# Optimization experiments

Hardware: AMD Instinct MI355X
Metric: run time of the kernel (lower is better)

## Reference

```python
import jax, jax.numpy as jnp
import numpy as np

EPS = 1e-5

def headwise_linear(x, w):
    # x: [B,S,D], w: [NH, DH_out, DH_in] block-diagonal linear per head
    B, S, D = x.shape
    NH, O, DH = w.shape
    xh = x.reshape(B, S, NH, DH)
    return jnp.einsum('bshd,hod->bsho', xh, w).reshape(B, S, NH * O)

def setup_inputs() -> dict:
    key = jax.random.key(0)
    ks = jax.random.split(key, 10)
    B, S, D, NH, K = 8, 4096, 768, 4, 4
    DH = D // NH
    small = (2.0 / (5.0 * D)) ** 0.5  # small_init scale
    return {
        'x': jax.random.normal(ks[0], (B, S, D), jnp.float32),
        'conv_w': jax.random.normal(ks[1], (D, 1, K), jnp.float32) * (1.0 / K ** 0.5),
        'conv_b': jnp.zeros((D,), jnp.float32),
        'w_f': jax.random.normal(ks[2], (NH, DH, DH), jnp.float32) * small,
        'w_i': jax.random.normal(ks[3], (NH, DH, DH), jnp.float32) * small,
        'w_z': jax.random.normal(ks[4], (NH, DH, DH), jnp.float32) * small,
        'w_o': jax.random.normal(ks[5], (NH, DH, DH), jnp.float32) * small,
        'r_kernel': jax.random.normal(ks[6], (NH, DH, 4, DH), jnp.float32) * (1.0 / DH ** 0.5),
        'r_bias': jnp.zeros((4, NH, DH), jnp.float32),
        'gn_weight': jnp.ones((D,), jnp.float32),
    }

def reference(x, conv_w, conv_b, w_f, w_i, w_z, w_o, r_kernel, r_bias, gn_weight):
    B, S, D = x.shape
    NH, DH = r_kernel.shape[0], r_kernel.shape[1]
    K = conv_w.shape[-1]
    # --- causal depthwise conv1d + SiLU ---
    xt = jnp.transpose(x, (0, 2, 1))  # [B,D,S]
    xc = jax.lax.conv_general_dilated(xt, conv_w, (1,), [(K - 1, 0)],
                                      feature_group_count=D)
    x_conv = jax.nn.silu(jnp.transpose(xc + conv_b[None, :, None], (0, 2, 1)))
    # --- headwise gate projections (note: original code feeds fgate->i, igate->f) ---
    gi = headwise_linear(x_conv, w_f)
    gf = headwise_linear(x_conv, w_i)
    gz = headwise_linear(x, w_z)
    go = headwise_linear(x, w_o)
    Wx = jnp.stack([gi, gf, gz, go], axis=2).reshape(B, S, 4, NH, DH)
    Wx = jnp.transpose(Wx, (1, 0, 2, 3, 4))  # [S,B,4,NH,DH]
    # --- sLSTM recurrent scan with exponential gating + stabilizer m ---
    def step(carry, wx_t):
        y, c, n, m = carry  # each [B,NH,DH]
        Ry = jnp.einsum('bhd,hdge->bghe', y, r_kernel)  # [B,4,NH,DH]
        raw = wx_t + Ry + r_bias[None]
        iraw, fraw, zraw, oraw = raw[:, 0], raw[:, 1], raw[:, 2], raw[:, 3]
        logfplusm = m + jax.nn.log_sigmoid(fraw)
        mnew = jnp.maximum(iraw, logfplusm)
        igate = jnp.exp(iraw - mnew)
        fgate = jnp.exp(logfplusm - mnew)
        cnew = fgate * c + igate * jnp.tanh(zraw)
        nnew = fgate * n + igate
        ynew = jax.nn.sigmoid(oraw) * cnew / nnew
        return (ynew, cnew, nnew, mnew), ynew
    init = tuple(jnp.zeros((B, NH, DH), x.dtype) for _ in range(4))
    _, ys = jax.lax.scan(step, init, Wx)  # [S,B,NH,DH]
    y = jnp.transpose(ys, (1, 2, 0, 3))  # [B,NH,S,DH]
    # --- multi-head layer norm (group norm with NH groups over DH) ---
    mean = y.mean(-1, keepdims=True)
    var = y.var(-1, keepdims=True)
    yn = (y - mean) * jax.lax.rsqrt(var + EPS)
    yn = yn * gn_weight.reshape(1, NH, 1, DH)
    return jnp.transpose(yn, (0, 2, 1, 3)).reshape(B, S, NH * DH)
```

## Files before the change

### kernel.cpp

```cpp
#include <hip/hip_runtime.h>
#include <hip/hip_bf16.h>
#include <math.h>

#define B_ 8
#define S_ 4096
#define D_ 768
#define NH_ 4
#define DH_ 192
#define NTOT_ 768

typedef __attribute__((ext_vector_type(8))) short short8;
typedef __attribute__((ext_vector_type(4))) float floatx4;
typedef __attribute__((ext_vector_type(4))) short short4v;
typedef __attribute__((ext_vector_type(4))) unsigned int uint4v;
typedef _Float16 f16;

__device__ __forceinline__ short f2bs(float f) {
  union { float f; unsigned u; } v; v.f = f;
  unsigned r = v.u + 0x7FFFu + ((v.u >> 16) & 1u);
  return (short)(r >> 16);
}
__device__ __forceinline__ float bs2f(unsigned short s) {
  union { unsigned u; float f; } v; v.u = ((unsigned)s) << 16;
  return v.f;
}
__device__ __forceinline__ unsigned packh2(float lo, float hi) {
  union { f16 h[2]; unsigned u; } x;
  x.h[0] = (f16)lo; x.h[1] = (f16)hi;
  return x.u;
}

__device__ __forceinline__ float DOT2(unsigned r, unsigned y, float acc) {
  asm("v_dot2_f32_f16 %0, %1, %2, %0" : "+v"(acc) : "v"(r), "v"(y));
  return acc;
}

template<int CTRL>
__device__ __forceinline__ float qperm(float x) {
  return __int_as_float(__builtin_amdgcn_mov_dpp(__float_as_int(x), CTRL, 0xf, 0xf, true));
}

__global__ __launch_bounds__(256) void wconv_kernel(
    const float* __restrict__ wf, const float* __restrict__ wi,
    const float* __restrict__ wz, const float* __restrict__ wo,
    short* __restrict__ Wbf)
{
  int idx = blockIdx.x * 256 + threadIdx.x;
  int hg = idx / (DH_ * DH_);
  int r  = idx % (DH_ * DH_);
  int h = hg >> 2, g = hg & 3;
  const float* W = (g == 0) ? wf : (g == 1) ? wi : (g == 2) ? wz : wo;
  Wbf[idx] = f2bs(W[(size_t)h * DH_ * DH_ + r]);
}

__global__ __launch_bounds__(256) void conv_silu_kernel(
    const float* __restrict__ x, const float* __restrict__ cw, const float* __restrict__ cb,
    short* __restrict__ xb, short* __restrict__ xcb)
{
  const int b  = blockIdx.x / (S_ / 64);
  const int s0 = (blockIdx.x % (S_ / 64)) * 64;
  const int tid = threadIdx.x;
  float wv[3][4], bias[3], win[3][3];
  for (int j = 0; j < 3; ++j) {
    int d = tid + j * 256;
    for (int k = 0; k < 4; ++k) wv[j][k] = cw[d * 4 + k];
    bias[j] = cb[d];
    for (int p = 0; p < 3; ++p) {
      int s = s0 - 3 + p;
      win[j][p] = (s >= 0) ? x[((size_t)b * S_ + s) * D_ + d] : 0.f;
    }
  }
  for (int i = 0; i < 64; ++i) {
    size_t base = ((size_t)b * S_ + (s0 + i)) * D_;
    for (int j = 0; j < 3; ++j) {
      int d = tid + j * 256;
      float xc = x[base + d];
      float a = bias[j] + win[j][0] * wv[j][0] + win[j][1] * wv[j][1]
                        + win[j][2] * wv[j][2] + xc * wv[j][3];
      float sv = a / (1.f + __expf(-a));
      xb[base + d]  = f2bs(xc);
      xcb[base + d] = f2bs(sv);
      win[j][0] = win[j][1]; win[j][1] = win[j][2]; win[j][2] = xc;
    }
  }
}

__global__ __launch_bounds__(256) void proj_kernel(
    const short* __restrict__ xb, const short* __restrict__ xcb,
    const short* __restrict__ Wbf, short* __restrict__ P)
{
  const int hg = blockIdx.y;
  const int h = hg >> 2, g = hg & 3;
  const short* A  = (g < 2) ? xcb : xb;
  const short* Wb = Wbf + (size_t)hg * (DH_ * DH_);
  const int tid = threadIdx.x, w = tid >> 6, l = tid & 63;
  const int l15 = l & 15, lg = l >> 4;
  const int R0 = blockIdx.x * 256 + w * 64;

  for (int mp = 0; mp < 2; ++mp) {
    const int rb0 = R0 + mp * 32;
    floatx4 acc[2][12];
    for (int u = 0; u < 2; ++u)
      for (int nt = 0; nt < 12; ++nt) acc[u][nt] = (floatx4){0.f, 0.f, 0.f, 0.f};
    const short* Ar = A + (size_t)(rb0 + l15) * D_ + h * DH_ + lg * 8;
    const short* Bp = Wb + l15 * DH_ + lg * 8;
    for (int kk = 0; kk < 6; ++kk) {
      short8 a0 = *(const short8*)(Ar + kk * 32);
      short8 a1 = *(const short8*)(Ar + (size_t)16 * D_ + kk * 32);
      for (int nt = 0; nt < 12; ++nt) {
        short8 bf = *(const short8*)(Bp + nt * 16 * DH_ + kk * 32);
        acc[0][nt] = __builtin_amdgcn_mfma_f32_16x16x32_bf16(a0, bf, acc[0][nt], 0, 0, 0);
        acc[1][nt] = __builtin_amdgcn_mfma_f32_16x16x32_bf16(a1, bf, acc[1][nt], 0, 0, 0);
      }
    }
    for (int u = 0; u < 2; ++u) {
      for (int q = 0; q < 4; ++q) {
        int row = rb0 + u * 16 + lg * 4 + q;
        int s = row & (S_ - 1);
        int bb = row >> 12;
        size_t ob = (((size_t)h * B_ + bb) * S_ + s) * NTOT_ + l15 * 4 + g;
        for (int nt = 0; nt < 12; ++nt) P[ob + nt * 64] = f2bs(acc[u][nt][q]);
      }
    }
  }
}

__global__ __launch_bounds__(768)
__attribute__((amdgpu_waves_per_eu(3, 3)))
void scan_kernel(short* P_, const float* __restrict__ rk, const float* __restrict__ rb)
{
  const int bid = blockIdx.x;
  const int h = bid >> 3;
  const int t0 = threadIdx.x;
  const int e = t0 >> 2, q = t0 & 3;

  __shared__ __align__(16) f16 y_lds[2][DH_];

  unsigned Rr[4][24];
  {
    const float* Rh = rk + (size_t)h * (DH_ * NTOT_);
#pragma unroll
    for (int j = 0; j < 24; ++j) {
      const int k0 = 48 * q + 2 * j;
#pragma unroll
      for (int g = 0; g < 4; ++g) {
        float v0 = Rh[((size_t)k0 * 4 + g) * DH_ + e];
        float v1 = Rh[((size_t)(k0 + 1) * 4 + g) * DH_ + e];
        Rr[g][j] = packh2(v0, v1);
      }
    }
  }
  float biasv[4];
#pragma unroll
  for (int g = 0; g < 4; ++g) biasv[g] = rb[(g * NH_ + h) * DH_ + e];

  if (t0 < DH_) y_lds[0][t0] = (f16)0.f;

  float c = 0.f, nrm = 0.f, m = 0.f;
  short* Pc = P_ + (size_t)bid * S_ * NTOT_;
  short4v wxc = *(const short4v*)(Pc + e * 4);
  __syncthreads();

#pragma unroll 1
  for (int t = 0; t < S_; ++t) {
    short4v wxn = {};
    if (t + 1 < S_) wxn = *(const short4v*)(Pc + (size_t)(t + 1) * NTOT_ + e * 4);

    const f16* yb = &y_lds[t & 1][q * 48];
    float a0 = 0.f, a1 = 0.f, a2 = 0.f, a3 = 0.f;
#pragma unroll
    for (int i = 0; i < 6; ++i) {
      uint4v yv = ((const uint4v*)yb)[i];
#pragma unroll
      for (int u = 0; u < 4; ++u) {
        const unsigned yp = yv[u];
        const int j = i * 4 + u;
        a0 = DOT2(Rr[0][j], yp, a0);
        a1 = DOT2(Rr[1][j], yp, a1);
        a2 = DOT2(Rr[2][j], yp, a2);
        a3 = DOT2(Rr[3][j], yp, a3);
      }
    }
    a0 += qperm<0xB1>(a0);  a0 += qperm<0x4E>(a0);
    a1 += qperm<0xB1>(a1);  a1 += qperm<0x4E>(a1);
    a2 += qperm<0xB1>(a2);  a2 += qperm<0x4E>(a2);
    a3 += qperm<0xB1>(a3);  a3 += qperm<0x4E>(a3);

    float ir  = bs2f((unsigned short)wxc[0]) + a0 + biasv[0];
    float fr  = bs2f((unsigned short)wxc[1]) + a1 + biasv[1];
    float zr  = bs2f((unsigned short)wxc[2]) + a2 + biasv[2];
    float orr = bs2f((unsigned short)wxc[3]) + a3 + biasv[3];

    float lsf = fminf(fr, 0.f) - __logf(1.f + __expf(-fabsf(fr)));
    float lfm = m + lsf;
    float mnew = fmaxf(ir, lfm);
    float ig = __expf(ir - mnew);
    float fg = __expf(lfm - mnew);
    float e2z = __expf(2.f * zr);
    float tz = 1.f - 2.f / (e2z + 1.f);
    c   = fg * c + ig * tz;
    nrm = fg * nrm + ig;
    m = mnew;
    float sg = 1.f / (1.f + __expf(-orr));
    float y = sg * c / nrm;

    f16 yh = (f16)y;
    if (q == 0) {
      y_lds[(t & 1) ^ 1][e] = yh;
      union { f16 hh; short ss; } uv; uv.hh = yh;
      Pc[(size_t)t * NTOT_ + e] = uv.ss;
    }
    wxc = wxn;
    __syncthreads();
  }
}

__global__ __launch_bounds__(256) void gnorm_kernel(
    const short* __restrict__ yws, const float* __restrict__ gnw,
    float* __restrict__ out)
{
  const int row = blockIdx.x * 4 + (threadIdx.x >> 6);
  const int l = threadIdx.x & 63;
  const int h = row >> 15;
  const int b = (row >> 12) & 7;
  const int s = row & (S_ - 1);
  const short* yr = yws + (size_t)row * NTOT_;
  float v[3];
  float su = 0.f, sq = 0.f;
#pragma unroll
  for (int j = 0; j < 3; ++j) {
    unsigned short u = (unsigned short)yr[l + j * 64];
    union { unsigned short u; f16 h; } cv; cv.u = u;
    v[j] = (float)cv.h;
    su += v[j]; sq += v[j] * v[j];
  }
  for (int off = 32; off; off >>= 1) {
    su += __shfl_xor(su, off);
    sq += __shfl_xor(sq, off);
  }
  float mean = su * (1.f / DH_);
  float var = sq * (1.f / DH_) - mean * mean;
  float rs = rsqrtf(var + 1e-5f);
  float* orow = out + ((size_t)b * S_ + s) * D_ + h * DH_;
#pragma unroll
  for (int j = 0; j < 3; ++j)
    orow[l + j * 64] = (v[j] - mean) * rs * gnw[h * DH_ + l + j * 64];
}

extern "C" void kernel_launch(void* const* d_in, const int* in_sizes, int n_in,
                              void* d_out, int out_size, void* d_ws, size_t ws_size,
                              hipStream_t stream) {
  const float* x   = (const float*)d_in[0];
  const float* cw  = (const float*)d_in[1];
  const float* cb  = (const float*)d_in[2];
  const float* wf  = (const float*)d_in[3];
  const float* wi  = (const float*)d_in[4];
  const float* wz  = (const float*)d_in[5];
  const float* wo  = (const float*)d_in[6];
  const float* rk  = (const float*)d_in[7];
  const float* rb  = (const float*)d_in[8];
  const float* gnw = (const float*)d_in[9];
  float* out = (float*)d_out;

  short* P   = (short*)d_ws;
  short* Wbf = (short*)((char*)d_ws + (size_t)201326592);
  short* xb  = (short*)d_out;
  short* xcb = (short*)((char*)d_out + (size_t)50331648);

  wconv_kernel<<<dim3(2304), 256, 0, stream>>>(wf, wi, wz, wo, Wbf);
  conv_silu_kernel<<<dim3(512), 256, 0, stream>>>(x, cw, cb, xb, xcb);
  proj_kernel<<<dim3(128, 16), 256, 0, stream>>>(xb, xcb, Wbf, P);
  scan_kernel<<<dim3(32), 768, 0, stream>>>(P, rk, rb);
  gnorm_kernel<<<dim3(32768), 256, 0, stream>>>(P, gnw, out);
}
```

Before: 5.665 ms.

## Repartition recurrent matvec across 1024 threads with LDS gate exchange

```diff
diff --git a/kernel.cpp b/kernel.cpp
--- a/kernel.cpp
+++ b/kernel.cpp
@@ -125,90 +125,102 @@
   }
 }
 
-__global__ __launch_bounds__(768)
-__attribute__((amdgpu_waves_per_eu(3, 3)))
-void scan_kernel(short* P_, const float* __restrict__ rk, const float* __restrict__ rb)
+__global__ __launch_bounds__(1024) void scan_kernel(
+    short* P_, const float* __restrict__ rk, const float* __restrict__ rb)
 {
   const int bid = blockIdx.x;
   const int h = bid >> 3;
-  const int t0 = threadIdx.x;
-  const int e = t0 >> 2, q = t0 & 3;
-
-  __shared__ __align__(16) f16 y_lds[2][DH_];
-
-  unsigned Rr[4][24];
+  const int tid = threadIdx.x;
+  const int Q = tid >> 2, u = tid & 3;
+  const int g = Q >> 6;
+  const int e3 = (Q & 63) * 3;
+
+  __shared__ __align__(16) f16 y_lds[DH_];
+  __shared__ __align__(16) float raw_lds[DH_][4];
+
+  unsigned Rr[3][24];
   {
     const float* Rh = rk + (size_t)h * (DH_ * NTOT_);
 #pragma unroll
-    for (int j = 0; j < 24; ++j) {
-      const int k0 = 48 * q + 2 * j;
-#pragma unroll
-      for (int g = 0; g < 4; ++g) {
-        float v0 = Rh[((size_t)k0 * 4 + g) * DH_ + e];
-        float v1 = Rh[((size_t)(k0 + 1) * 4 + g) * DH_ + e];
-        Rr[g][j] = packh2(v0, v1);
-      }
-    }
-  }
-  float biasv[4];
-#pragma unroll
-  for (int g = 0; g < 4; ++g) biasv[g] = rb[(g * NH_ + h) * DH_ + e];
-
-  if (t0 < DH_) y_lds[0][t0] = (f16)0.f;
+    for (int j = 0; j < 3; ++j) {
+#pragma unroll
+      for (int m = 0; m < 24; ++m) {
+        const int k0 = 48 * u + 2 * m;
+        float v0 = Rh[((size_t)k0 * 4 + g) * DH_ + e3 + j];
+        float v1 = Rh[((size_t)(k0 + 1) * 4 + g) * DH_ + e3 + j];
+        Rr[j][m] = packh2(v0, v1);
+      }
+    }
+  }
+
+  float biasv[4] = {0.f, 0.f, 0.f, 0.f};
+  if (tid < NTOT_) {
+#pragma unroll
+    for (int gg = 0; gg < 4; ++gg) biasv[gg] = rb[(gg * NH_ + h) * DH_ + Q];
+  }
+  if (tid < DH_) y_lds[tid] = (f16)0.f;
 
   float c = 0.f, nrm = 0.f, m = 0.f;
   short* Pc = P_ + (size_t)bid * S_ * NTOT_;
-  short4v wxc = *(const short4v*)(Pc + e * 4);
+  short4v wxc = {};
+  if (tid < NTOT_) wxc = *(const short4v*)(Pc + Q * 4);
   __syncthreads();
 
 #pragma unroll 1
   for (int t = 0; t < S_; ++t) {
     short4v wxn = {};
-    if (t + 1 < S_) wxn = *(const short4v*)(Pc + (size_t)(t + 1) * NTOT_ + e * 4);
-
-    const f16* yb = &y_lds[t & 1][q * 48];
-    float a0 = 0.f, a1 = 0.f, a2 = 0.f, a3 = 0.f;
+    if (tid < NTOT_ && t + 1 < S_)
+      wxn = *(const short4v*)(Pc + (size_t)(t + 1) * NTOT_ + Q * 4);
+
+    const f16* yb = y_lds + 48 * u;
+    float a0 = 0.f, a1 = 0.f, a2 = 0.f;
 #pragma unroll
     for (int i = 0; i < 6; ++i) {
       uint4v yv = ((const uint4v*)yb)[i];
 #pragma unroll
-      for (int u = 0; u < 4; ++u) {
-        const unsigned yp = yv[u];
-        const int j = i * 4 + u;
+      for (int mm = 0; mm < 4; ++mm) {
+        const unsigned yp = yv[mm];
+        const int j = i * 4 + mm;
         a0 = DOT2(Rr[0][j], yp, a0);
         a1 = DOT2(Rr[1][j], yp, a1);
         a2 = DOT2(Rr[2][j], yp, a2);
-        a3 = DOT2(Rr[3][j], yp, a3);
       }
     }
     a0 += qperm<0xB1>(a0);  a0 += qperm<0x4E>(a0);
     a1 += qperm<0xB1>(a1);  a1 += qperm<0x4E>(a1);
     a2 += qperm<0xB1>(a2);  a2 += qperm<0x4E>(a2);
-    a3 += qperm<0xB1>(a3);  a3 += qperm<0x4E>(a3);
-
-    float ir  = bs2f((unsigned short)wxc[0]) + a0 + biasv[0];
-    float fr  = bs2f((unsigned short)wxc[1]) + a1 + biasv[1];
-    float zr  = bs2f((unsigned short)wxc[2]) + a2 + biasv[2];
-    float orr = bs2f((unsigned short)wxc[3]) + a3 + biasv[3];
-
-    float lsf = fminf(fr, 0.f) - __logf(1.f + __expf(-fabsf(fr)));
-    float lfm = m + lsf;
-    float mnew = fmaxf(ir, lfm);
-    float ig = __expf(ir - mnew);
-    float fg = __expf(lfm - mnew);
-    float e2z = __expf(2.f * zr);
-    float tz = 1.f - 2.f / (e2z + 1.f);
-    c   = fg * c + ig * tz;
-    nrm = fg * nrm + ig;
-    m = mnew;
-    float sg = 1.f / (1.f + __expf(-orr));
-    float y = sg * c / nrm;
-
-    f16 yh = (f16)y;
-    if (q == 0) {
-      y_lds[(t & 1) ^ 1][e] = yh;
-      union { f16 hh; short ss; } uv; uv.hh = yh;
-      Pc[(size_t)t * NTOT_ + e] = uv.ss;
+    if (u < 3) {
+      float av = (u == 0) ? a0 : (u == 1) ? a1 : a2;
+      raw_lds[e3 + u][g] = av;
+    }
+    __syncthreads();
+
+    if (tid < NTOT_) {
+      floatx4 r4 = *(const floatx4*)raw_lds[Q];
+      float ir  = bs2f((unsigned short)wxc[0]) + r4[0] + biasv[0];
+      float fr  = bs2f((unsigned short)wxc[1]) + r4[1] + biasv[1];
+      float zr  = bs2f((unsigned short)wxc[2]) + r4[2] + biasv[2];
+      float orr = bs2f((unsigned short)wxc[3]) + r4[3] + biasv[3];
+
+      float lsf = fminf(fr, 0.f) - __logf(1.f + __expf(-fabsf(fr)));
+      float lfm = m + lsf;
+      float mnew = fmaxf(ir, lfm);
+      float ig = __expf(ir - mnew);
+      float fg = __expf(lfm - mnew);
+      float e2z = __expf(2.f * zr);
+      float tz = 1.f - 2.f / (e2z + 1.f);
+      c   = fg * c + ig * tz;
+      nrm = fg * nrm + ig;
+      m = mnew;
+      float sg = 1.f / (1.f + __expf(-orr));
+      float y = sg * c / nrm;
+
+      if (u == 0) {
+        f16 yh = (f16)y;
+        y_lds[Q] = yh;
+        union { f16 hh; short ss; } uv; uv.hh = yh;
+        Pc[(size_t)t * NTOT_ + Q] = uv.ss;
+      }
     }
     wxc = wxn;
     __syncthreads();
@@ -270,6 +282,6 @@
   wconv_kernel<<<dim3(2304), 256, 0, stream>>>(wf, wi, wz, wo, Wbf);
   conv_silu_kernel<<<dim3(512), 256, 0, stream>>>(x, cw, cb, xb, xcb);
   proj_kernel<<<dim3(128, 16), 256, 0, stream>>>(xb, xcb, Wbf, P);
-  scan_kernel<<<dim3(32), 768, 0, stream>>>(P, rk, rb);
+  scan_kernel<<<dim3(32), 1024, 0, stream>>>(P, rk, rb);
   gnorm_kernel<<<dim3(32768), 256, 0, stream>>>(P, gnw, out);
 }
```

After: 6.051 ms. 1.07x slower.

## Move half of recurrent weights to LDS, fold bias into projection, use fast reciprocals

Applied to the files above, without the earlier changes.

```diff
diff --git a/kernel.cpp b/kernel.cpp
--- a/kernel.cpp
+++ b/kernel.cpp
@@ -87,7 +87,8 @@
 
 __global__ __launch_bounds__(256) void proj_kernel(
     const short* __restrict__ xb, const short* __restrict__ xcb,
-    const short* __restrict__ Wbf, short* __restrict__ P)
+    const short* __restrict__ Wbf, const float* __restrict__ rb,
+    short* __restrict__ P)
 {
   const int hg = blockIdx.y;
   const int h = hg >> 2, g = hg & 3;
@@ -96,6 +97,11 @@
   const int tid = threadIdx.x, w = tid >> 6, l = tid & 63;
   const int l15 = l & 15, lg = l >> 4;
   const int R0 = blockIdx.x * 256 + w * 64;
+
+  float rbv[12];
+#pragma unroll
+  for (int nt = 0; nt < 12; ++nt)
+    rbv[nt] = rb[(g * NH_ + h) * DH_ + l15 + nt * 16];
 
   for (int mp = 0; mp < 2; ++mp) {
     const int rb0 = R0 + mp * 32;
@@ -119,66 +125,82 @@
         int s = row & (S_ - 1);
         int bb = row >> 12;
         size_t ob = (((size_t)h * B_ + bb) * S_ + s) * NTOT_ + l15 * 4 + g;
-        for (int nt = 0; nt < 12; ++nt) P[ob + nt * 64] = f2bs(acc[u][nt][q]);
+        for (int nt = 0; nt < 12; ++nt)
+          P[ob + nt * 64] = f2bs(acc[u][nt][q] + rbv[nt]);
       }
     }
   }
 }
 
+#define RL_BYTES 147456
+#define CHUNK_B  12288
 __global__ __launch_bounds__(768)
-__attribute__((amdgpu_waves_per_eu(3, 3)))
-void scan_kernel(short* P_, const float* __restrict__ rk, const float* __restrict__ rb)
+void scan_kernel(short* P_, const float* __restrict__ rk)
 {
   const int bid = blockIdx.x;
   const int h = bid >> 3;
   const int t0 = threadIdx.x;
   const int e = t0 >> 2, q = t0 & 3;
 
-  __shared__ __align__(16) f16 y_lds[2][DH_];
-
-  unsigned Rr[4][24];
-  {
-    const float* Rh = rk + (size_t)h * (DH_ * NTOT_);
-#pragma unroll
-    for (int j = 0; j < 24; ++j) {
-      const int k0 = 48 * q + 2 * j;
-#pragma unroll
-      for (int g = 0; g < 4; ++g) {
-        float v0 = Rh[((size_t)k0 * 4 + g) * DH_ + e];
-        float v1 = Rh[((size_t)(k0 + 1) * 4 + g) * DH_ + e];
-        Rr[g][j] = packh2(v0, v1);
-      }
-    }
-  }
-  float biasv[4];
-#pragma unroll
-  for (int g = 0; g < 4; ++g) biasv[g] = rb[(g * NH_ + h) * DH_ + e];
-
-  if (t0 < DH_) y_lds[0][t0] = (f16)0.f;
+  __shared__ __align__(16) char shbuf[RL_BYTES + 2 * DH_ * 2];
+  f16* ybuf = (f16*)(shbuf + RL_BYTES);
+
+  const float* Rh = rk + (size_t)h * (DH_ * NTOT_);
+
+  unsigned Rr[2][24];
+#pragma unroll
+  for (int j = 0; j < 24; ++j) {
+    const int k0 = 48 * q + 2 * j;
+#pragma unroll
+    for (int g = 0; g < 2; ++g) {
+      float v0 = Rh[((size_t)k0 * 4 + g) * DH_ + e];
+      float v1 = Rh[((size_t)(k0 + 1) * 4 + g) * DH_ + e];
+      Rr[g][j] = packh2(v0, v1);
+    }
+  }
+#pragma unroll
+  for (int c = 0; c < 12; ++c) {
+    const int gate = 2 + (c >= 6);
+    const int m0 = (c % 6) * 4;
+    uint4v blk;
+#pragma unroll
+    for (int j = 0; j < 4; ++j) {
+      const int k0 = 48 * q + 2 * (m0 + j);
+      blk[j] = packh2(Rh[((size_t)k0 * 4 + gate) * DH_ + e],
+                      Rh[((size_t)(k0 + 1) * 4 + gate) * DH_ + e]);
+    }
+    *(uint4v*)(shbuf + c * CHUNK_B + t0 * 16) = blk;
+  }
+
+  if (t0 < DH_) ybuf[t0] = (f16)0.f;
 
   float c = 0.f, nrm = 0.f, m = 0.f;
   short* Pc = P_ + (size_t)bid * S_ * NTOT_;
   short4v wxc = *(const short4v*)(Pc + e * 4);
   __syncthreads();
 
+  const char* rlz = shbuf + t0 * 16;
+  const char* rlo = rlz + 6 * CHUNK_B;
+
 #pragma unroll 1
   for (int t = 0; t < S_; ++t) {
     short4v wxn = {};
     if (t + 1 < S_) wxn = *(const short4v*)(Pc + (size_t)(t + 1) * NTOT_ + e * 4);
 
-    const f16* yb = &y_lds[t & 1][q * 48];
+    const f16* yb = ybuf + (t & 1) * DH_ + q * 48;
     float a0 = 0.f, a1 = 0.f, a2 = 0.f, a3 = 0.f;
 #pragma unroll
     for (int i = 0; i < 6; ++i) {
-      uint4v yv = ((const uint4v*)yb)[i];
+      uint4v Y = *(const uint4v*)(yb + i * 8);
+      uint4v Z = *(const uint4v*)(rlz + i * CHUNK_B);
+      uint4v O = *(const uint4v*)(rlo + i * CHUNK_B);
 #pragma unroll
       for (int u = 0; u < 4; ++u) {
-        const unsigned yp = yv[u];
         const int j = i * 4 + u;
-        a0 = DOT2(Rr[0][j], yp, a0);
-        a1 = DOT2(Rr[1][j], yp, a1);
-        a2 = DOT2(Rr[2][j], yp, a2);
-        a3 = DOT2(Rr[3][j], yp, a3);
+        a0 = DOT2(Rr[0][j], Y[u], a0);
+        a1 = DOT2(Rr[1][j], Y[u], a1);
+        a2 = DOT2(Z[u], Y[u], a2);
+        a3 = DOT2(O[u], Y[u], a3);
       }
     }
     a0 += qperm<0xB1>(a0);  a0 += qperm<0x4E>(a0);
@@ -186,10 +208,10 @@
     a2 += qperm<0xB1>(a2);  a2 += qperm<0x4E>(a2);
     a3 += qperm<0xB1>(a3);  a3 += qperm<0x4E>(a3);
 
-    float ir  = bs2f((unsigned short)wxc[0]) + a0 + biasv[0];
-    float fr  = bs2f((unsigned short)wxc[1]) + a1 + biasv[1];
-    float zr  = bs2f((unsigned short)wxc[2]) + a2 + biasv[2];
-    float orr = bs2f((unsigned short)wxc[3]) + a3 + biasv[3];
+    float ir  = bs2f((unsigned short)wxc[0]) + a0;
+    float fr  = bs2f((unsigned short)wxc[1]) + a1;
+    float zr  = bs2f((unsigned short)wxc[2]) + a2;
+    float orr = bs2f((unsigned short)wxc[3]) + a3;
 
     float lsf = fminf(fr, 0.f) - __logf(1.f + __expf(-fabsf(fr)));
     float lfm = m + lsf;
@@ -197,16 +219,16 @@
     float ig = __expf(ir - mnew);
     float fg = __expf(lfm - mnew);
     float e2z = __expf(2.f * zr);
-    float tz = 1.f - 2.f / (e2z + 1.f);
+    float tz = 1.f - 2.f * __builtin_amdgcn_rcpf(e2z + 1.f);
     c   = fg * c + ig * tz;
     nrm = fg * nrm + ig;
     m = mnew;
-    float sg = 1.f / (1.f + __expf(-orr));
-    float y = sg * c / nrm;
+    float sg = __builtin_amdgcn_rcpf(1.f + __expf(-orr));
+    float y = sg * c * __builtin_amdgcn_rcpf(nrm);
 
     f16 yh = (f16)y;
     if (q == 0) {
-      y_lds[(t & 1) ^ 1][e] = yh;
+      ybuf[((t & 1) ^ 1) * DH_ + e] = yh;
       union { f16 hh; short ss; } uv; uv.hh = yh;
       Pc[(size_t)t * NTOT_ + e] = uv.ss;
     }
@@ -269,7 +291,7 @@
 
   wconv_kernel<<<dim3(2304), 256, 0, stream>>>(wf, wi, wz, wo, Wbf);
   conv_silu_kernel<<<dim3(512), 256, 0, stream>>>(x, cw, cb, xb, xcb);
-  proj_kernel<<<dim3(128, 16), 256, 0, stream>>>(xb, xcb, Wbf, P);
-  scan_kernel<<<dim3(32), 768, 0, stream>>>(P, rk, rb);
+  proj_kernel<<<dim3(128, 16), 256, 0, stream>>>(xb, xcb, Wbf, rb, P);
+  scan_kernel<<<dim3(32), 768, 0, stream>>>(P, rk);
   gnorm_kernel<<<dim3(32768), 256, 0, stream>>>(P, gnw, out);
 }
```

Measured after the change: 4.955 ms. 1.14x faster.
